# Performance work log

Hardware: AMD Instinct MI355X
Metric: run time of the kernel (lower is better)

Reference implementation:

```python
import jax, jax.numpy as jnp
import numpy as np
import math

D_MODEL = 1024
N_DEVICES = 64
HIDDEN = 128
N_HEADS = 8
B, S = 16, 1024
W_SCALE = 0.02

def setup_inputs() -> dict:
    key = jax.random.key(0)
    ks = jax.random.split(key, 24)
    f = jax.random.normal
    inp = {
        'x': f(ks[0], (B, S, D_MODEL), jnp.float32),
        # attention pooling (n_heads=8, non-causal, self-attention) weights, stored [in,out]
        'wq': f(ks[1], (D_MODEL, D_MODEL), jnp.float32) * W_SCALE,
        'bq': jnp.zeros((D_MODEL,), jnp.float32),
        'wk': f(ks[2], (D_MODEL, D_MODEL), jnp.float32) * W_SCALE,
        'bk': jnp.zeros((D_MODEL,), jnp.float32),
        'wv': f(ks[3], (D_MODEL, D_MODEL), jnp.float32) * W_SCALE,
        'bv': jnp.zeros((D_MODEL,), jnp.float32),
        'wo': f(ks[4], (D_MODEL, D_MODEL), jnp.float32) * W_SCALE,
        'bo': jnp.zeros((D_MODEL,), jnp.float32),
        # device embedding table
        'emb': f(ks[5], (N_DEVICES, D_MODEL), jnp.float32),
        # routing gate: Linear(2d,d) -> Tanh -> Linear(d,N) -> Softmax
        'rg_w1': f(ks[6], (2 * D_MODEL, D_MODEL), jnp.float32) * W_SCALE,
        'rg_b1': jnp.zeros((D_MODEL,), jnp.float32),
        'rg_w2': f(ks[7], (D_MODEL, N_DEVICES), jnp.float32) * W_SCALE,
        'rg_b2': jnp.zeros((N_DEVICES,), jnp.float32),
        'reg_w1': f(ks[8], (N_DEVICES, D_MODEL, HIDDEN), jnp.float32) * W_SCALE,
        'reg_b1': jnp.zeros((N_DEVICES, HIDDEN), jnp.float32),
        'reg_w2': f(ks[9], (N_DEVICES, HIDDEN), jnp.float32) * W_SCALE,
        'reg_b2': jnp.zeros((N_DEVICES,), jnp.float32),
        # stacked per-device classification heads: Linear(d,h)->ReLU->Linear(h,1)->Sigmoid
        'cls_w1': f(ks[10], (N_DEVICES, D_MODEL, HIDDEN), jnp.float32) * W_SCALE,
        'cls_b1': jnp.zeros((N_DEVICES, HIDDEN), jnp.float32),
        'cls_w2': f(ks[11], (N_DEVICES, HIDDEN), jnp.float32) * W_SCALE,
        'cls_b2': jnp.zeros((N_DEVICES,), jnp.float32),
    }
    return inp


def _forward(x, wq, bq, wk, bk, wv, bv, wo, bo, emb,
             rg_w1, rg_b1, rg_w2, rg_b2,
             reg_w1, reg_b1, reg_w2, reg_b2,
             cls_w1, cls_b1, cls_w2, cls_b2):
    b, s, d = x.shape
    dk = d // N_HEADS
    scale = 1.0 / math.sqrt(dk)

    def split_heads(t):  # [b,s,d] -> [b,h,s,dk]
        return t.reshape(b, s, N_HEADS, dk).transpose(0, 2, 1, 3)

    Q = split_heads(x @ wq + bq)
    K = split_heads(x @ wk + bk)
    V = split_heads(x @ wv + bv)
    scores = jnp.einsum('bhqd,bhkd->bhqk', Q, K) * scale
    attn = jax.nn.softmax(scores, axis=-1)  # non-causal, no mask, eval (no dropout)
    ctx = jnp.einsum('bhqk,bhkd->bhqd', attn, V)
    ctx = ctx.transpose(0, 2, 1, 3).reshape(b, s, d)
    pooled = ctx @ wo + bo                       # [b,s,d]
    g = pooled.mean(axis=1)                      # [b,d] global_repr

    g_exp = jnp.broadcast_to(g[:, None, :], (b, N_DEVICES, d))
    de_exp = jnp.broadcast_to(emb[None, :, :], (b, N_DEVICES, d))

    # routing gate
    ri = jnp.concatenate([g_exp, de_exp], axis=-1)        # [b,N,2d]
    h = jnp.tanh(ri @ rg_w1 + rg_b1)                      # [b,N,d]
    rw = jax.nn.softmax(h @ rg_w2 + rg_b2, axis=-1)       # [b,N,N]
    device_repr = jnp.einsum('bnm,md->bnd', rw, emb)      # bmm with expanded embeds
    combined = g_exp + device_repr                        # [b,N,d]

    hr = jax.nn.relu(jnp.einsum('bnd,ndh->bnh', combined, reg_w1) + reg_b1)
    reg = jax.nn.softplus(jnp.einsum('bnh,nh->bn', hr, reg_w2) + reg_b2)

    # per-device classification heads (stacked)
    hc = jax.nn.relu(jnp.einsum('bnd,ndh->bnh', combined, cls_w1) + cls_b1)
    cls = jax.nn.sigmoid(jnp.einsum('bnh,nh->bn', hc, cls_w2) + cls_b2)
    return reg, cls


def reference(x, wq, bq, wk, bk, wv, bv, wo, bo, emb,
              rg_w1, rg_b1, rg_w2, rg_b2,
              reg_w1, reg_b1, reg_w2, reg_b2,
              cls_w1, cls_b1, cls_w2, cls_b2):
    return _forward(x, wq, bq, wk, bk, wv, bv, wo, bo, emb,
                    rg_w1, rg_b1, rg_w2, rg_b2,
                    reg_w1, reg_b1, reg_w2, reg_b2,
                    cls_w1, cls_b1, cls_w2, cls_b2)
```

## Files before the change

kernel.cpp:

```cpp
#include <hip/hip_runtime.h>

typedef unsigned short ushort_t;
typedef __attribute__((ext_vector_type(8))) short short8;
typedef __attribute__((ext_vector_type(4))) float floatx4;

__device__ __forceinline__ ushort_t f2bf(float f) {
    unsigned u = __float_as_uint(f);
    return (ushort_t)((u + 0x7fffu + ((u >> 16) & 1u)) >> 16);
}
__device__ __forceinline__ void gll16(const void* g, void* l) {
    __builtin_amdgcn_global_load_lds(
        (const __attribute__((address_space(1))) unsigned int*)g,
        (__attribute__((address_space(3))) unsigned int*)l, 16, 0, 0);
}
#if __has_builtin(__builtin_amdgcn_exp2f)
#define EXP2f(x) __builtin_amdgcn_exp2f(x)
#else
#define EXP2f(x) exp2f(x)
#endif

__global__ __launch_bounds__(256) void prep_tr_kernel(
    const float* __restrict__ x, ushort_t* __restrict__ xb,
    const float* __restrict__ wq, const float* __restrict__ wk,
    ushort_t* __restrict__ wqT, ushort_t* __restrict__ wkT)
{
    __shared__ float t[64][65];
    const int bid = blockIdx.x;
    const int tid = threadIdx.x;
    if (bid < 8192) {
        size_t i = ((size_t)bid * 256 + tid) * 8;
        float4 v0 = *(const float4*)(x + i);
        float4 v1 = *(const float4*)(x + i + 4);
        uint4 o;
        o.x = (unsigned)f2bf(v0.x) | ((unsigned)f2bf(v0.y) << 16);
        o.y = (unsigned)f2bf(v0.z) | ((unsigned)f2bf(v0.w) << 16);
        o.z = (unsigned)f2bf(v1.x) | ((unsigned)f2bf(v1.y) << 16);
        o.w = (unsigned)f2bf(v1.z) | ((unsigned)f2bf(v1.w) << 16);
        *(uint4*)(xb + i) = o;
        return;
    }
    const int b2 = bid - 8192;
    const int bx = b2 & 15, by = (b2 >> 4) & 15, bz = b2 >> 8;
    const float* src = bz ? wk : wq;
    ushort_t* dst = bz ? wkT : wqT;
    const int k0 = bx * 64, n0 = by * 64;
    const int rr = tid >> 4, cc = (tid & 15) * 4;
#pragma unroll
    for (int p = 0; p < 4; ++p) {
        float4 v = *(const float4*)(src + (size_t)(k0 + p * 16 + rr) * 1024 + n0 + cc);
        t[p * 16 + rr][cc + 0] = v.x;
        t[p * 16 + rr][cc + 1] = v.y;
        t[p * 16 + rr][cc + 2] = v.z;
        t[p * 16 + rr][cc + 3] = v.w;
    }
    __syncthreads();
#pragma unroll
    for (int p = 0; p < 4; ++p) {
        int nl = p * 16 + rr;
        uint2 o;
        o.x = (unsigned)f2bf(t[cc + 0][nl]) | ((unsigned)f2bf(t[cc + 1][nl]) << 16);
        o.y = (unsigned)f2bf(t[cc + 2][nl]) | ((unsigned)f2bf(t[cc + 3][nl]) << 16);
        *(uint2*)(dst + (size_t)(n0 + nl) * 1024 + k0 + cc) = o;
    }
}

__global__ __launch_bounds__(512, 4) void gemm_qk_kernel(
    const ushort_t* __restrict__ xb, const ushort_t* __restrict__ wqT, const ushort_t* __restrict__ wkT,
    const float* __restrict__ bq, const float* __restrict__ bk,
    ushort_t* __restrict__ Qb, ushort_t* __restrict__ Kb)
{
    const int bm = blockIdx.x;
    const int bn = blockIdx.y;

    __shared__ ushort_t a_lds[2][128 * 32];
    __shared__ ushort_t q_lds[2][128 * 32];
    __shared__ ushort_t k_lds[2][128 * 32];

    const int tid = threadIdx.x;
    const int lane = tid & 63;
    const int wave = tid >> 6;
    const int wmat = wave >> 2;
    const int wr = (wave >> 1) & 1, wc = wave & 1;
    const int l16 = lane & 15, quad = lane >> 4;
    const int qs = quad ^ ((l16 >> 1) & 3);

    floatx4 acc[4][4];
    const floatx4 zero4 = {0.f, 0.f, 0.f, 0.f};
#pragma unroll
    for (int i = 0; i < 4; ++i)
#pragma unroll
        for (int j = 0; j < 4; ++j) acc[i][j] = zero4;

    const int srow = tid >> 2;
    const int skof = ((tid & 3) ^ ((tid >> 3) & 3)) * 8;
    const ushort_t* gA = xb + (size_t)(bm * 128 + srow) * 1024 + skof;
    const ushort_t* gQ = wqT + (size_t)(bn * 128 + srow) * 1024 + skof;
    const ushort_t* gK = wkT + (size_t)(bn * 128 + srow) * 1024 + skof;

    auto issue = [&](int buf, int k0) {
        gll16(gA + k0, &a_lds[buf][wave * 512]);
        gll16(gQ + k0, &q_lds[buf][wave * 512]);
        gll16(gK + k0, &k_lds[buf][wave * 512]);
    };

    const ushort_t* lbase = wmat ? k_lds[0] : q_lds[0];
    const int lstride = wmat ? (int)(k_lds[1] - k_lds[0]) : (int)(q_lds[1] - q_lds[0]);

    auto compute = [&](int buf) {
        const ushort_t* la = a_lds[buf];
        const ushort_t* lb = lbase + buf * lstride;
        short8 afr[4], bfr[4];
#pragma unroll
        for (int mi = 0; mi < 4; ++mi)
            afr[mi] = *(const short8*)&la[(wr * 64 + mi * 16 + l16) * 32 + qs * 8];
#pragma unroll
        for (int ni = 0; ni < 4; ++ni)
            bfr[ni] = *(const short8*)&lb[(wc * 64 + ni * 16 + l16) * 32 + qs * 8];
#pragma unroll
        for (int mi = 0; mi < 4; ++mi)
#pragma unroll
            for (int ni = 0; ni < 4; ++ni)
                acc[mi][ni] = __builtin_amdgcn_mfma_f32_16x16x32_bf16(afr[mi], bfr[ni], acc[mi][ni], 0, 0, 0);
    };

    issue(0, 0);
#pragma unroll 4
    for (int kt = 0; kt < 31; ++kt) {
        __syncthreads();
        issue((kt + 1) & 1, (kt + 1) * 32);
        compute(kt & 1);
    }
    __syncthreads();
    compute(1);

    ushort_t* Out = wmat ? Kb : Qb;
    const float* bias = wmat ? bk : bq;
    const float postscale = wmat ? 1.0f : 0.12751744900508692f;

    const int bq_ = bm >> 3;
    const int sb = (bm & 7) * 128 + wr * 64 + quad * 4;
    const int dc = wc * 64 + l16;
    float bp[4];
#pragma unroll
    for (int ni = 0; ni < 4; ++ni) bp[ni] = bias[bn * 128 + dc + ni * 16] * postscale;
    ushort_t* ob = Out + ((size_t)(bq_ * 8 + bn) * 1024 + sb) * 128 + dc;
#pragma unroll
    for (int mi = 0; mi < 4; ++mi)
#pragma unroll
        for (int ni = 0; ni < 4; ++ni) {
            ushort_t* p = ob + mi * 2048 + ni * 16;
#pragma unroll
            for (int r = 0; r < 4; ++r)
                p[r * 128] = f2bf(fmaf(acc[mi][ni][r], postscale, bp[ni]));
        }
}

__global__ __launch_bounds__(512, 4) void attn_mfma_kernel(
    const ushort_t* __restrict__ Qb,
    const ushort_t* __restrict__ Kb,
    float* __restrict__ wout)
{
    const int bh = blockIdx.x;
    const int qt = blockIdx.y;
    __shared__ ushort_t ks[2][64 * 128];

    const int tid = threadIdx.x;
    const int wave = tid >> 6, lane = tid & 63;
    const int l16 = lane & 15, quad = lane >> 4;

    const ushort_t* Ksrc = Kb + (size_t)bh * 1024 * 128;

    int srcoff[2];
#pragma unroll
    for (int c = 0; c < 2; ++c) {
        int r = c * 32 + (tid >> 4);
        int g = (tid & 15) ^ (r & 15);
        srcoff[c] = r * 128 + g * 8;
    }

    auto issue = [&](int buf, int kt) {
        const ushort_t* src = Ksrc + (size_t)kt * 8192;
#pragma unroll
        for (int c = 0; c < 2; ++c)
            gll16(src + srcoff[c], &ks[buf][c * 4096 + wave * 512]);
    };

    short8 aq[2][4];
    {
        const ushort_t* qsrc = Qb + ((size_t)bh * 1024 + qt * 256 + wave * 32) * 128;
#pragma unroll
        for (int mi = 0; mi < 2; ++mi)
#pragma unroll
            for (int ksp = 0; ksp < 4; ++ksp)
                aq[mi][ksp] = *(const short8*)(qsrc + (size_t)(mi * 16 + l16) * 128 + ksp * 32 + quad * 8);
    }

    const floatx4 zero4 = {0.f, 0.f, 0.f, 0.f};
    float lsum[2][4];
#pragma unroll
    for (int mi = 0; mi < 2; ++mi)
#pragma unroll
        for (int r = 0; r < 4; ++r) lsum[mi][r] = 0.f;

    issue(0, 0);

    for (int kt = 0; kt < 16; ++kt) {
        __syncthreads();
        if (kt < 15) issue((kt + 1) & 1, kt + 1);
        const ushort_t* kbuf = ks[kt & 1];
        floatx4 acc[2][4];
#pragma unroll
        for (int mi = 0; mi < 2; ++mi)
#pragma unroll
            for (int ni = 0; ni < 4; ++ni) acc[mi][ni] = zero4;
#pragma unroll
        for (int ksp = 0; ksp < 4; ++ksp) {
            short8 bk[4];
#pragma unroll
            for (int ni = 0; ni < 4; ++ni) {
                int n = ni * 16 + l16;
                int gs = (ksp * 4 + quad) ^ (n & 15);
                bk[ni] = *(const short8*)&kbuf[n * 128 + gs * 8];
            }
#pragma unroll
            for (int mi = 0; mi < 2; ++mi)
#pragma unroll
                for (int ni = 0; ni < 4; ++ni)
                    acc[mi][ni] = __builtin_amdgcn_mfma_f32_16x16x32_bf16(aq[mi][ksp], bk[ni], acc[mi][ni], 0, 0, 0);
        }
#pragma unroll
        for (int mi = 0; mi < 2; ++mi)
#pragma unroll
            for (int r = 0; r < 4; ++r) {
                float s = 0.f;
#pragma unroll
                for (int ni = 0; ni < 4; ++ni) s += EXP2f(acc[mi][ni][r]);
                lsum[mi][r] += s;
            }
    }

    issue(0, 0);

    float invl[2][4];
#pragma unroll
    for (int mi = 0; mi < 2; ++mi)
#pragma unroll
        for (int r = 0; r < 4; ++r) {
            float s = lsum[mi][r];
#pragma unroll
            for (int off = 1; off < 16; off <<= 1) s += __shfl_xor(s, off, 16);
            invl[mi][r] = 1.f / s;
        }

    for (int kt = 0; kt < 16; ++kt) {
        __syncthreads();
        if (kt < 15) issue((kt + 1) & 1, kt + 1);
        const ushort_t* kbuf = ks[kt & 1];
        floatx4 acc[2][4];
#pragma unroll
        for (int mi = 0; mi < 2; ++mi)
#pragma unroll
            for (int ni = 0; ni < 4; ++ni) acc[mi][ni] = zero4;
#pragma unroll
        for (int ksp = 0; ksp < 4; ++ksp) {
            short8 bk[4];
#pragma unroll
            for (int ni = 0; ni < 4; ++ni) {
                int n = ni * 16 + l16;
                int gs = (ksp * 4 + quad) ^ (n & 15);
                bk[ni] = *(const short8*)&kbuf[n * 128 + gs * 8];
            }
#pragma unroll
            for (int mi = 0; mi < 2; ++mi)
#pragma unroll
                for (int ni = 0; ni < 4; ++ni)
                    acc[mi][ni] = __builtin_amdgcn_mfma_f32_16x16x32_bf16(aq[mi][ksp], bk[ni], acc[mi][ni], 0, 0, 0);
        }
#pragma unroll
        for (int ni = 0; ni < 4; ++ni) {
            float s = 0.f;
#pragma unroll
            for (int mi = 0; mi < 2; ++mi)
#pragma unroll
                for (int r = 0; r < 4; ++r)
                    s += EXP2f(acc[mi][ni][r]) * invl[mi][r];
            s += __shfl_xor(s, 16, 64);
            s += __shfl_xor(s, 32, 64);
            if (quad == 0) atomicAdd(&wout[bh * 1024 + kt * 64 + ni * 16 + l16], s);
        }
    }
}

__global__ __launch_bounds__(256) void u_kernel(const ushort_t* __restrict__ xb,
                                                const float* __restrict__ w,
                                                float* __restrict__ u)
{
    const int b = blockIdx.x, dc = blockIdx.y;
    const int tid = threadIdx.x;
    const int kp = tid >> 4, dli = tid & 15;
    const int d0 = dc * 64;
    __shared__ float4 accl[16][8][16];

    float4 acc[8];
#pragma unroll
    for (int h = 0; h < 8; ++h) acc[h] = make_float4(0.f, 0.f, 0.f, 0.f);

    const ushort_t* Xp = xb + ((size_t)(b * 1024 + kp * 64)) * 1024 + d0 + dli * 4;
    const float* wb = w + b * 8192 + kp * 64;
    for (int k = 0; k < 64; ++k) {
        uint2 uv = *(const uint2*)(Xp + (size_t)k * 1024);
        float x0 = __uint_as_float(uv.x << 16);
        float x1 = __uint_as_float(uv.x & 0xffff0000u);
        float x2 = __uint_as_float(uv.y << 16);
        float x3 = __uint_as_float(uv.y & 0xffff0000u);
#pragma unroll
        for (int h = 0; h < 8; ++h) {
            float ww = wb[h * 1024 + k];
            acc[h].x = fmaf(ww, x0, acc[h].x);
            acc[h].y = fmaf(ww, x1, acc[h].y);
            acc[h].z = fmaf(ww, x2, acc[h].z);
            acc[h].w = fmaf(ww, x3, acc[h].w);
        }
    }
#pragma unroll
    for (int h = 0; h < 8; ++h) accl[kp][h][dli] = acc[h];
    __syncthreads();
    if (tid < 128) {
        const int h = tid >> 4, di = tid & 15;
        float4 s = accl[0][h][di];
#pragma unroll
        for (int k2 = 1; k2 < 16; ++k2) {
            float4 v = accl[k2][h][di];
            s.x += v.x; s.y += v.y; s.z += v.z; s.w += v.w;
        }
        *(float4*)&u[((size_t)(b * 8 + h)) * 1024 + d0 + di * 4] = s;
    }
}

__global__ __launch_bounds__(256) void sgemm_kernel(
    const float* __restrict__ A, int lda, long sAz,
    const float* __restrict__ Bm, int ldb, long sBz,
    const float* __restrict__ bias, long sBiasz,
    float* __restrict__ C, int ldc, long sCz,
    int M, int N, int K, float alpha, int nks)
{
    const int z = blockIdx.z;
    const int ks = blockIdx.x % nks;
    const int mt = blockIdx.x / nks;
    const int Kc = K / nks;
    A += (size_t)z * sAz;
    Bm += (size_t)z * sBz;
    C += (size_t)z * sCz;
    const float* bptr = bias ? bias + (size_t)z * sBiasz : nullptr;
    __shared__ float As[64 * 36];
    __shared__ float Bs[32 * 68];
    const int tid = threadIdx.x;
    const int row0 = mt * 64, col0 = blockIdx.y * 64;
    const int ty = tid >> 4, tx = tid & 15;
    float acc[4][4] = {};
    const int aflat = tid * 8;
    const int ar = aflat >> 5, ac = aflat & 31;
    const int br = aflat >> 6, bc = aflat & 63;
    for (int k0 = ks * Kc; k0 < (ks + 1) * Kc; k0 += 32) {
        __syncthreads();
        float4 va0 = make_float4(0.f, 0.f, 0.f, 0.f), va1 = va0;
        if (row0 + ar < M) {
            const float* src = A + (size_t)(row0 + ar) * lda + k0 + ac;
            va0 = *(const float4*)src;
            va1 = *(const float4*)(src + 4);
        }
        *(float4*)&As[ar * 36 + ac] = va0;
        *(float4*)&As[ar * 36 + ac + 4] = va1;
        {
            const float* srcb = Bm + (size_t)(k0 + br) * ldb + col0 + bc;
            *(float4*)&Bs[br * 68 + bc] = *(const float4*)srcb;
            *(float4*)&Bs[br * 68 + bc + 4] = *(const float4*)(srcb + 4);
        }
        __syncthreads();
#pragma unroll
        for (int kk = 0; kk < 32; ++kk) {
            float a0 = As[(ty * 4 + 0) * 36 + kk];
            float a1 = As[(ty * 4 + 1) * 36 + kk];
            float a2 = As[(ty * 4 + 2) * 36 + kk];
            float a3 = As[(ty * 4 + 3) * 36 + kk];
            float b0 = Bs[kk * 68 + tx * 4 + 0];
            float b1 = Bs[kk * 68 + tx * 4 + 1];
            float b2 = Bs[kk * 68 + tx * 4 + 2];
            float b3 = Bs[kk * 68 + tx * 4 + 3];
            acc[0][0] = fmaf(a0, b0, acc[0][0]); acc[0][1] = fmaf(a0, b1, acc[0][1]);
            acc[0][2] = fmaf(a0, b2, acc[0][2]); acc[0][3] = fmaf(a0, b3, acc[0][3]);
            acc[1][0] = fmaf(a1, b0, acc[1][0]); acc[1][1] = fmaf(a1, b1, acc[1][1]);
            acc[1][2] = fmaf(a1, b2, acc[1][2]); acc[1][3] = fmaf(a1, b3, acc[1][3]);
            acc[2][0] = fmaf(a2, b0, acc[2][0]); acc[2][1] = fmaf(a2, b1, acc[2][1]);
            acc[2][2] = fmaf(a2, b2, acc[2][2]); acc[2][3] = fmaf(a2, b3, acc[2][3]);
            acc[3][0] = fmaf(a3, b0, acc[3][0]); acc[3][1] = fmaf(a3, b1, acc[3][1]);
            acc[3][2] = fmaf(a3, b2, acc[3][2]); acc[3][3] = fmaf(a3, b3, acc[3][3]);
        }
    }
#pragma unroll
    for (int i = 0; i < 4; ++i) {
        int r = row0 + ty * 4 + i;
        if (r >= M) continue;
#pragma unroll
        for (int j = 0; j < 4; ++j) {
            int c = col0 + tx * 4 + j;
            float v = alpha * acc[i][j] + ((bptr && ks == 0) ? bptr[c] : 0.f);
            if (nks > 1) atomicAdd(&C[(size_t)r * ldc + c], v);
            else C[(size_t)r * ldc + c] = v;
        }
    }
}

__global__ __launch_bounds__(256) void sgemm_ge_ee_kernel(
    const float* __restrict__ gbuf, const float* __restrict__ emb,
    const float* __restrict__ rg_w1, float* __restrict__ Ge, float* __restrict__ Ee)
{
    const int z = blockIdx.z;
    const float* A = z ? emb : gbuf;
    const float* Bm = rg_w1 + (size_t)z * 1048576;
    float* C = z ? Ee : Ge;
    const int M = z ? 64 : 16;
    const int nks = 8, Kc = 128;
    const int ks = blockIdx.x % nks;
    __shared__ float As[64 * 36];
    __shared__ float Bs[32 * 68];
    const int tid = threadIdx.x;
    const int col0 = blockIdx.y * 64;
    const int ty = tid >> 4, tx = tid & 15;
    float acc[4][4] = {};
    const int aflat = tid * 8;
    const int ar = aflat >> 5, ac = aflat & 31;
    const int br = aflat >> 6, bc = aflat & 63;
    for (int k0 = ks * Kc; k0 < (ks + 1) * Kc; k0 += 32) {
        __syncthreads();
        float4 va0 = make_float4(0.f, 0.f, 0.f, 0.f), va1 = va0;
        if (ar < M) {
            const float* src = A + (size_t)ar * 1024 + k0 + ac;
            va0 = *(const float4*)src;
            va1 = *(const float4*)(src + 4);
        }
        *(float4*)&As[ar * 36 + ac] = va0;
        *(float4*)&As[ar * 36 + ac + 4] = va1;
        {
            const float* srcb = Bm + (size_t)(k0 + br) * 1024 + col0 + bc;
            *(float4*)&Bs[br * 68 + bc] = *(const float4*)srcb;
            *(float4*)&Bs[br * 68 + bc + 4] = *(const float4*)(srcb + 4);
        }
        __syncthreads();
#pragma unroll
        for (int kk = 0; kk < 32; ++kk) {
            float a0 = As[(ty * 4 + 0) * 36 + kk];
            float a1 = As[(ty * 4 + 1) * 36 + kk];
            float a2 = As[(ty * 4 + 2) * 36 + kk];
            float a3 = As[(ty * 4 + 3) * 36 + kk];
            float b0 = Bs[kk * 68 + tx * 4 + 0];
            float b1 = Bs[kk * 68 + tx * 4 + 1];
            float b2 = Bs[kk * 68 + tx * 4 + 2];
            float b3 = Bs[kk * 68 + tx * 4 + 3];
            acc[0][0] = fmaf(a0, b0, acc[0][0]); acc[0][1] = fmaf(a0, b1, acc[0][1]);
            acc[0][2] = fmaf(a0, b2, acc[0][2]); acc[0][3] = fmaf(a0, b3, acc[0][3]);
            acc[1][0] = fmaf(a1, b0, acc[1][0]); acc[1][1] = fmaf(a1, b1, acc[1][1]);
            acc[1][2] = fmaf(a1, b2, acc[1][2]); acc[1][3] = fmaf(a1, b3, acc[1][3]);
            acc[2][0] = fmaf(a2, b0, acc[2][0]); acc[2][1] = fmaf(a2, b1, acc[2][1]);
            acc[2][2] = fmaf(a2, b2, acc[2][2]); acc[2][3] = fmaf(a2, b3, acc[2][3]);
            acc[3][0] = fmaf(a3, b0, acc[3][0]); acc[3][1] = fmaf(a3, b1, acc[3][1]);
            acc[3][2] = fmaf(a3, b2, acc[3][2]); acc[3][3] = fmaf(a3, b3, acc[3][3]);
        }
    }
#pragma unroll
    for (int i = 0; i < 4; ++i) {
        int r = ty * 4 + i;
        if (r >= M) continue;
#pragma unroll
        for (int j = 0; j < 4; ++j) {
            int c = col0 + tx * 4 + j;
            atomicAdd(&C[(size_t)r * 1024 + c], acc[i][j]);
        }
    }
}

__global__ __launch_bounds__(256) void gate_kernel(
    const float* __restrict__ Ge, const float* __restrict__ Ee, const float* __restrict__ rg_b1,
    const float* __restrict__ rg_w2, const float* __restrict__ rg_b2,
    const float* __restrict__ emb, float* __restrict__ DR)
{
    const int row = blockIdx.x;
    const int b = row >> 6, n = row & 63;
    __shared__ float h[1024];
    __shared__ float red[256];
    __shared__ float rw[64];
    const int tid = threadIdx.x;
    for (int c = tid; c < 1024; c += 256)
        h[c] = tanhf(Ge[b * 1024 + c] + Ee[n * 1024 + c] + rg_b1[c]);
    __syncthreads();
    const int j = tid & 63, ch = tid >> 6;
    float part = 0.f;
    const float* w2p = rg_w2 + (size_t)(ch * 256) * 64 + j;
    for (int c = 0; c < 256; ++c)
        part = fmaf(h[ch * 256 + c], w2p[c * 64], part);
    red[tid] = part;
    __syncthreads();
    if (tid < 64) {
        float lg = red[tid] + red[tid + 64] + red[tid + 128] + red[tid + 192] + rg_b2[j];
        float m = lg;
#pragma unroll
        for (int off = 1; off < 64; off <<= 1) m = fmaxf(m, __shfl_xor(m, off, 64));
        float e = __expf(lg - m);
        float s = e;
#pragma unroll
        for (int off = 1; off < 64; off <<= 1) s += __shfl_xor(s, off, 64);
        rw[tid] = e / s;
    }
    __syncthreads();
    float4 acc = make_float4(0.f, 0.f, 0.f, 0.f);
    const float4* E4 = (const float4*)emb;
    for (int nn = 0; nn < 64; ++nn) {
        float wv = rw[nn];
        float4 ev = E4[nn * 256 + tid];
        acc.x = fmaf(wv, ev.x, acc.x);
        acc.y = fmaf(wv, ev.y, acc.y);
        acc.z = fmaf(wv, ev.z, acc.z);
        acc.w = fmaf(wv, ev.w, acc.w);
    }
    *(float4*)&DR[(size_t)row * 1024 + tid * 4] = acc;
}

__global__ __launch_bounds__(256) void heads_kernel(
    const float* __restrict__ g, const float* __restrict__ DR,
    const float* __restrict__ rw1, const float* __restrict__ cw1,
    const float* __restrict__ rb1, const float* __restrict__ rw2, const float* __restrict__ rb2,
    const float* __restrict__ cb1, const float* __restrict__ cw2, const float* __restrict__ cb2,
    float* __restrict__ out)
{
    const int n = blockIdx.x, task = blockIdx.y, bq = blockIdx.z;
    __shared__ float comb[4][1024];
    __shared__ float apart[2][4][128];
    const int tid = threadIdx.x;
#pragma unroll
    for (int i = 0; i < 4; ++i) {
        int idx = tid + i * 256;
        int bb = idx >> 8, c4 = idx & 255;
        int b = bq * 4 + bb;
        float4 gv = *(const float4*)&g[b * 1024 + c4 * 4];
        float4 dv = *(const float4*)&DR[((size_t)(b * 64 + n)) * 1024 + c4 * 4];
        *(float4*)&comb[bb][c4 * 4] = make_float4(gv.x + dv.x, gv.y + dv.y, gv.z + dv.z, gv.w + dv.w);
    }
    __syncthreads();
    const int j = tid & 127, sub = tid >> 7;
    const float* W1 = (task ? cw1 : rw1) + (size_t)n * 131072 + (size_t)sub * 512 * 128 + j;
    float a[4] = {};
    for (int c4 = 0; c4 < 128; ++c4) {
        const int cb = sub * 512 + c4 * 4;
        const float w0 = W1[(c4 * 4 + 0) * 128];
        const float w1 = W1[(c4 * 4 + 1) * 128];
        const float w2 = W1[(c4 * 4 + 2) * 128];
        const float w3 = W1[(c4 * 4 + 3) * 128];
#pragma unroll
        for (int bb = 0; bb < 4; ++bb) {
            float4 cv = *(const float4*)&comb[bb][cb];
            a[bb] = fmaf(cv.x, w0, a[bb]);
            a[bb] = fmaf(cv.y, w1, a[bb]);
            a[bb] = fmaf(cv.z, w2, a[bb]);
            a[bb] = fmaf(cv.w, w3, a[bb]);
        }
    }
#pragma unroll
    for (int bb = 0; bb < 4; ++bb) apart[sub][bb][j] = a[bb];
    __syncthreads();
    const int wv = tid >> 6, lane = tid & 63;
    const float* b1 = (task ? cb1 : rb1) + n * 128;
    const float* W2 = (task ? cw2 : rw2) + n * 128;
    float h1 = b1[lane]      + apart[0][wv][lane]      + apart[1][wv][lane];
    float h2 = b1[lane + 64] + apart[0][wv][lane + 64] + apart[1][wv][lane + 64];
    float s = fmaxf(h1, 0.f) * W2[lane] + fmaxf(h2, 0.f) * W2[lane + 64];
#pragma unroll
    for (int off = 1; off < 64; off <<= 1) s += __shfl_xor(s, off, 64);
    if (lane == 0) {
        s += (task ? cb2 : rb2)[n];
        float r = task ? (1.f / (1.f + __expf(-s)))
                       : (fmaxf(s, 0.f) + log1pf(__expf(-fabsf(s))));
        out[task * 1024 + (bq * 4 + wv) * 64 + n] = r;
    }
}

extern "C" void kernel_launch(void* const* d_in, const int* in_sizes, int n_in,
                              void* d_out, int out_size, void* d_ws, size_t ws_size,
                              hipStream_t stream)
{
    const float* x      = (const float*)d_in[0];
    const float* wq     = (const float*)d_in[1];
    const float* bq     = (const float*)d_in[2];
    const float* wk     = (const float*)d_in[3];
    const float* bk     = (const float*)d_in[4];
    const float* wv     = (const float*)d_in[5];
    const float* bv     = (const float*)d_in[6];
    const float* wo     = (const float*)d_in[7];
    const float* bo     = (const float*)d_in[8];
    const float* emb    = (const float*)d_in[9];
    const float* rg_w1  = (const float*)d_in[10];
    const float* rg_b1  = (const float*)d_in[11];
    const float* rg_w2  = (const float*)d_in[12];
    const float* rg_b2  = (const float*)d_in[13];
    const float* reg_w1 = (const float*)d_in[14];
    const float* reg_b1 = (const float*)d_in[15];
    const float* reg_w2 = (const float*)d_in[16];
    const float* reg_b2 = (const float*)d_in[17];
    const float* cls_w1 = (const float*)d_in[18];
    const float* cls_b1 = (const float*)d_in[19];
    const float* cls_w2 = (const float*)d_in[20];
    const float* cls_b2 = (const float*)d_in[21];

    char* ws = (char*)d_ws;
    size_t off = 0;
    auto alloc = [&](size_t bytes) { size_t cur = off; off += (bytes + 255) & ~(size_t)255; return cur; };

    ushort_t* xb  = (ushort_t*)(ws + alloc((size_t)16777216 * 2));
    ushort_t* wqT = (ushort_t*)(ws + alloc((size_t)1048576 * 2));
    ushort_t* wkT = (ushort_t*)(ws + alloc((size_t)1048576 * 2));
    ushort_t* Qb  = (ushort_t*)(ws + alloc((size_t)16777216 * 2));
    ushort_t* Kb  = (ushort_t*)(ws + alloc((size_t)16777216 * 2));
    size_t zero_beg = off;
    float* wcol = (float*)(ws + alloc((size_t)131072 * 4));
    float* cm   = (float*)(ws + alloc((size_t)16384 * 4));
    float* gbuf = (float*)(ws + alloc((size_t)16384 * 4));
    float* Ge   = (float*)(ws + alloc((size_t)16384 * 4));
    float* Ee   = (float*)(ws + alloc((size_t)65536 * 4));
    size_t zero_end = off;
    float* u    = (float*)(ws + alloc((size_t)131072 * 4));
    float* DR   = (float*)(ws + alloc((size_t)1048576 * 4));

    hipMemsetAsync(ws + zero_beg, 0, zero_end - zero_beg, stream);

    prep_tr_kernel<<<8704, 256, 0, stream>>>(x, xb, wq, wk, wqT, wkT);
    gemm_qk_kernel<<<dim3(128, 8), 512, 0, stream>>>(xb, wqT, wkT, bq, bk, Qb, Kb);
    attn_mfma_kernel<<<dim3(128, 4), 512, 0, stream>>>(Qb, Kb, wcol);
    u_kernel<<<dim3(16, 16), 256, 0, stream>>>(xb, wcol, u);
    sgemm_kernel<<<dim3(8, 2, 8), 256, 0, stream>>>(u, 8192, 1024, wv, 1024, 128, bv, 128,
                                                    cm, 1024, 128, 16, 128, 1024, 1.f / 1024.f, 8);
    sgemm_kernel<<<dim3(8, 16, 1), 256, 0, stream>>>(cm, 1024, 0, wo, 1024, 0, bo, 0,
                                                     gbuf, 1024, 0, 16, 1024, 1024, 1.f, 8);
    sgemm_ge_ee_kernel<<<dim3(8, 16, 2), 256, 0, stream>>>(gbuf, emb, rg_w1, Ge, Ee);
    gate_kernel<<<1024, 256, 0, stream>>>(Ge, Ee, rg_b1, rg_w2, rg_b2, emb, DR);
    heads_kernel<<<dim3(64, 2, 4), 256, 0, stream>>>(gbuf, DR, reg_w1, cls_w1,
                                                     reg_b1, reg_w2, reg_b2,
                                                     cls_b1, cls_w2, cls_b2, (float*)d_out);
    (void)in_sizes; (void)n_in; (void)out_size; (void)ws_size;
}
```

Measured before the change: 452.8 us.

## Hoist embedding-gate GEMM into prep kernel and batch gate rows per block

The emb @ rg_w1[d:] GEMM does not depend on the attention path, so it moves into the prep kernel as extra blocks and runs alongside the conversion and transpose work. The remaining Ge GEMM uses the generic sgemm kernel. The gate kernel now handles four rows per block, so each rg_w2 and emb load is reused four times and the grid shrinks from 1024 to 256 blocks. In exchange the prep kernel uses more shared memory and the gate kernel runs fewer blocks.

After: 451.6 us. Within noise of the previous version (-0.3%).

```diff
diff --git a/kernel.cpp b/kernel.cpp
--- a/kernel.cpp
+++ b/kernel.cpp
@@ -19,12 +19,74 @@
 #define EXP2f(x) exp2f(x)
 #endif
 
+
+__device__ __forceinline__ void sgemm_body(
+    const float* __restrict__ A, int lda, const float* __restrict__ Bm, int ldb,
+    const float* __restrict__ bias, float* __restrict__ C, int ldc,
+    int M, int Kc, int ks, int col0, float alpha,
+    int tid, float* As, float* Bs)
+{
+    const int ty = tid >> 4, tx = tid & 15;
+    float acc[4][4] = {};
+    const int aflat = tid * 8;
+    const int ar = aflat >> 5, ac = aflat & 31;
+    const int br = aflat >> 6, bc = aflat & 63;
+    for (int k0 = ks * Kc; k0 < (ks + 1) * Kc; k0 += 32) {
+        __syncthreads();
+        float4 va0 = make_float4(0.f, 0.f, 0.f, 0.f), va1 = va0;
+        if (ar < M) {
+            const float* src = A + (size_t)ar * lda + k0 + ac;
+            va0 = *(const float4*)src;
+            va1 = *(const float4*)(src + 4);
+        }
+        *(float4*)&As[ar * 36 + ac] = va0;
+        *(float4*)&As[ar * 36 + ac + 4] = va1;
+        {
+            const float* srcb = Bm + (size_t)(k0 + br) * ldb + col0 + bc;
+            *(float4*)&Bs[br * 68 + bc] = *(const float4*)srcb;
+            *(float4*)&Bs[br * 68 + bc + 4] = *(const float4*)(srcb + 4);
+        }
+        __syncthreads();
+#pragma unroll
+        for (int kk = 0; kk < 32; ++kk) {
+            float a0 = As[(ty * 4 + 0) * 36 + kk];
+            float a1 = As[(ty * 4 + 1) * 36 + kk];
+            float a2 = As[(ty * 4 + 2) * 36 + kk];
+            float a3 = As[(ty * 4 + 3) * 36 + kk];
+            float b0 = Bs[kk * 68 + tx * 4 + 0];
+            float b1 = Bs[kk * 68 + tx * 4 + 1];
+            float b2 = Bs[kk * 68 + tx * 4 + 2];
+            float b3 = Bs[kk * 68 + tx * 4 + 3];
+            acc[0][0] = fmaf(a0, b0, acc[0][0]); acc[0][1] = fmaf(a0, b1, acc[0][1]);
+            acc[0][2] = fmaf(a0, b2, acc[0][2]); acc[0][3] = fmaf(a0, b3, acc[0][3]);
+            acc[1][0] = fmaf(a1, b0, acc[1][0]); acc[1][1] = fmaf(a1, b1, acc[1][1]);
+            acc[1][2] = fmaf(a1, b2, acc[1][2]); acc[1][3] = fmaf(a1, b3, acc[1][3]);
+            acc[2][0] = fmaf(a2, b0, acc[2][0]); acc[2][1] = fmaf(a2, b1, acc[2][1]);
+            acc[2][2] = fmaf(a2, b2, acc[2][2]); acc[2][3] = fmaf(a2, b3, acc[2][3]);
+            acc[3][0] = fmaf(a3, b0, acc[3][0]); acc[3][1] = fmaf(a3, b1, acc[3][1]);
+            acc[3][2] = fmaf(a3, b2, acc[3][2]); acc[3][3] = fmaf(a3, b3, acc[3][3]);
+        }
+    }
+#pragma unroll
+    for (int i = 0; i < 4; ++i) {
+        int r = ty * 4 + i;
+        if (r >= M) continue;
+#pragma unroll
+        for (int j = 0; j < 4; ++j) {
+            int c = col0 + tx * 4 + j;
+            float v = alpha * acc[i][j] + ((bias && ks == 0) ? bias[c] : 0.f);
+            atomicAdd(&C[(size_t)r * ldc + c], v);
+        }
+    }
+}
+
 __global__ __launch_bounds__(256) void prep_tr_kernel(
     const float* __restrict__ x, ushort_t* __restrict__ xb,
     const float* __restrict__ wq, const float* __restrict__ wk,
-    ushort_t* __restrict__ wqT, ushort_t* __restrict__ wkT)
-{
-    __shared__ float t[64][65];
+    ushort_t* __restrict__ wqT, ushort_t* __restrict__ wkT,
+    const float* __restrict__ emb, const float* __restrict__ rg_w1, float* __restrict__ Ee)
+{
+    __shared__ __align__(16) char psm[18432];
     const int bid = blockIdx.x;
     const int tid = threadIdx.x;
     if (bid < 8192) {
@@ -39,29 +101,39 @@
         *(uint4*)(xb + i) = o;
         return;
     }
-    const int b2 = bid - 8192;
-    const int bx = b2 & 15, by = (b2 >> 4) & 15, bz = b2 >> 8;
-    const float* src = bz ? wk : wq;
-    ushort_t* dst = bz ? wkT : wqT;
-    const int k0 = bx * 64, n0 = by * 64;
-    const int rr = tid >> 4, cc = (tid & 15) * 4;
-#pragma unroll
-    for (int p = 0; p < 4; ++p) {
-        float4 v = *(const float4*)(src + (size_t)(k0 + p * 16 + rr) * 1024 + n0 + cc);
-        t[p * 16 + rr][cc + 0] = v.x;
-        t[p * 16 + rr][cc + 1] = v.y;
-        t[p * 16 + rr][cc + 2] = v.z;
-        t[p * 16 + rr][cc + 3] = v.w;
-    }
-    __syncthreads();
-#pragma unroll
-    for (int p = 0; p < 4; ++p) {
-        int nl = p * 16 + rr;
-        uint2 o;
-        o.x = (unsigned)f2bf(t[cc + 0][nl]) | ((unsigned)f2bf(t[cc + 1][nl]) << 16);
-        o.y = (unsigned)f2bf(t[cc + 2][nl]) | ((unsigned)f2bf(t[cc + 3][nl]) << 16);
-        *(uint2*)(dst + (size_t)(n0 + nl) * 1024 + k0 + cc) = o;
-    }
+    if (bid < 8704) {
+        float (*t)[65] = (float(*)[65])psm;
+        const int b2 = bid - 8192;
+        const int bx = b2 & 15, by = (b2 >> 4) & 15, bz = b2 >> 8;
+        const float* src = bz ? wk : wq;
+        ushort_t* dst = bz ? wkT : wqT;
+        const int k0 = bx * 64, n0 = by * 64;
+        const int rr = tid >> 4, cc = (tid & 15) * 4;
+#pragma unroll
+        for (int p = 0; p < 4; ++p) {
+            float4 v = *(const float4*)(src + (size_t)(k0 + p * 16 + rr) * 1024 + n0 + cc);
+            t[p * 16 + rr][cc + 0] = v.x;
+            t[p * 16 + rr][cc + 1] = v.y;
+            t[p * 16 + rr][cc + 2] = v.z;
+            t[p * 16 + rr][cc + 3] = v.w;
+        }
+        __syncthreads();
+#pragma unroll
+        for (int p = 0; p < 4; ++p) {
+            int nl = p * 16 + rr;
+            uint2 o;
+            o.x = (unsigned)f2bf(t[cc + 0][nl]) | ((unsigned)f2bf(t[cc + 1][nl]) << 16);
+            o.y = (unsigned)f2bf(t[cc + 2][nl]) | ((unsigned)f2bf(t[cc + 3][nl]) << 16);
+            *(uint2*)(dst + (size_t)(n0 + nl) * 1024 + k0 + cc) = o;
+        }
+        return;
+    }
+    float* As = (float*)psm;
+    float* Bs = As + 64 * 36;
+    const int bx2 = bid - 8704;
+    const int ks = bx2 & 7, coly = bx2 >> 3;
+    sgemm_body(emb, 1024, rg_w1 + (size_t)1048576, 1024, nullptr,
+               Ee, 1024, 64, 128, ks, coly * 64, 1.f, tid, As, Bs);
 }
 
 __global__ __launch_bounds__(512, 4) void gemm_qk_kernel(
@@ -411,118 +483,67 @@
     }
 }
 
-__global__ __launch_bounds__(256) void sgemm_ge_ee_kernel(
-    const float* __restrict__ gbuf, const float* __restrict__ emb,
-    const float* __restrict__ rg_w1, float* __restrict__ Ge, float* __restrict__ Ee)
-{
-    const int z = blockIdx.z;
-    const float* A = z ? emb : gbuf;
-    const float* Bm = rg_w1 + (size_t)z * 1048576;
-    float* C = z ? Ee : Ge;
-    const int M = z ? 64 : 16;
-    const int nks = 8, Kc = 128;
-    const int ks = blockIdx.x % nks;
-    __shared__ float As[64 * 36];
-    __shared__ float Bs[32 * 68];
-    const int tid = threadIdx.x;
-    const int col0 = blockIdx.y * 64;
-    const int ty = tid >> 4, tx = tid & 15;
-    float acc[4][4] = {};
-    const int aflat = tid * 8;
-    const int ar = aflat >> 5, ac = aflat & 31;
-    const int br = aflat >> 6, bc = aflat & 63;
-    for (int k0 = ks * Kc; k0 < (ks + 1) * Kc; k0 += 32) {
-        __syncthreads();
-        float4 va0 = make_float4(0.f, 0.f, 0.f, 0.f), va1 = va0;
-        if (ar < M) {
-            const float* src = A + (size_t)ar * 1024 + k0 + ac;
-            va0 = *(const float4*)src;
-            va1 = *(const float4*)(src + 4);
-        }
-        *(float4*)&As[ar * 36 + ac] = va0;
-        *(float4*)&As[ar * 36 + ac + 4] = va1;
-        {
-            const float* srcb = Bm + (size_t)(k0 + br) * 1024 + col0 + bc;
-            *(float4*)&Bs[br * 68 + bc] = *(const float4*)srcb;
-            *(float4*)&Bs[br * 68 + bc + 4] = *(const float4*)(srcb + 4);
-        }
-        __syncthreads();
-#pragma unroll
-        for (int kk = 0; kk < 32; ++kk) {
-            float a0 = As[(ty * 4 + 0) * 36 + kk];
-            float a1 = As[(ty * 4 + 1) * 36 + kk];
-            float a2 = As[(ty * 4 + 2) * 36 + kk];
-            float a3 = As[(ty * 4 + 3) * 36 + kk];
-            float b0 = Bs[kk * 68 + tx * 4 + 0];
-            float b1 = Bs[kk * 68 + tx * 4 + 1];
-            float b2 = Bs[kk * 68 + tx * 4 + 2];
-            float b3 = Bs[kk * 68 + tx * 4 + 3];
-            acc[0][0] = fmaf(a0, b0, acc[0][0]); acc[0][1] = fmaf(a0, b1, acc[0][1]);
-            acc[0][2] = fmaf(a0, b2, acc[0][2]); acc[0][3] = fmaf(a0, b3, acc[0][3]);
-            acc[1][0] = fmaf(a1, b0, acc[1][0]); acc[1][1] = fmaf(a1, b1, acc[1][1]);
-            acc[1][2] = fmaf(a1, b2, acc[1][2]); acc[1][3] = fmaf(a1, b3, acc[1][3]);
-            acc[2][0] = fmaf(a2, b0, acc[2][0]); acc[2][1] = fmaf(a2, b1, acc[2][1]);
-            acc[2][2] = fmaf(a2, b2, acc[2][2]); acc[2][3] = fmaf(a2, b3, acc[2][3]);
-            acc[3][0] = fmaf(a3, b0, acc[3][0]); acc[3][1] = fmaf(a3, b1, acc[3][1]);
-            acc[3][2] = fmaf(a3, b2, acc[3][2]); acc[3][3] = fmaf(a3, b3, acc[3][3]);
-        }
-    }
-#pragma unroll
-    for (int i = 0; i < 4; ++i) {
-        int r = ty * 4 + i;
-        if (r >= M) continue;
-#pragma unroll
-        for (int j = 0; j < 4; ++j) {
-            int c = col0 + tx * 4 + j;
-            atomicAdd(&C[(size_t)r * 1024 + c], acc[i][j]);
-        }
-    }
-}
-
 __global__ __launch_bounds__(256) void gate_kernel(
     const float* __restrict__ Ge, const float* __restrict__ Ee, const float* __restrict__ rg_b1,
     const float* __restrict__ rg_w2, const float* __restrict__ rg_b2,
     const float* __restrict__ emb, float* __restrict__ DR)
 {
-    const int row = blockIdx.x;
-    const int b = row >> 6, n = row & 63;
-    __shared__ float h[1024];
-    __shared__ float red[256];
-    __shared__ float rw[64];
+    const int row0 = blockIdx.x * 4;
+    const int b = row0 >> 6, n0 = row0 & 63;
+    __shared__ float h[4][1024];
+    __shared__ float red[4][256];
+    __shared__ float rw[4][64];
     const int tid = threadIdx.x;
-    for (int c = tid; c < 1024; c += 256)
-        h[c] = tanhf(Ge[b * 1024 + c] + Ee[n * 1024 + c] + rg_b1[c]);
+    for (int idx = tid; idx < 4096; idx += 256) {
+        int rr = idx >> 10, c = idx & 1023;
+        h[rr][c] = tanhf(Ge[b * 1024 + c] + Ee[(n0 + rr) * 1024 + c] + rg_b1[c]);
+    }
     __syncthreads();
     const int j = tid & 63, ch = tid >> 6;
-    float part = 0.f;
+    float part[4] = {0.f, 0.f, 0.f, 0.f};
     const float* w2p = rg_w2 + (size_t)(ch * 256) * 64 + j;
-    for (int c = 0; c < 256; ++c)
-        part = fmaf(h[ch * 256 + c], w2p[c * 64], part);
-    red[tid] = part;
+    for (int c = 0; c < 256; ++c) {
+        float w = w2p[c * 64];
+#pragma unroll
+        for (int rr = 0; rr < 4; ++rr)
+            part[rr] = fmaf(h[rr][ch * 256 + c], w, part[rr]);
+    }
+#pragma unroll
+    for (int rr = 0; rr < 4; ++rr) red[rr][tid] = part[rr];
     __syncthreads();
     if (tid < 64) {
-        float lg = red[tid] + red[tid + 64] + red[tid + 128] + red[tid + 192] + rg_b2[j];
-        float m = lg;
-#pragma unroll
-        for (int off = 1; off < 64; off <<= 1) m = fmaxf(m, __shfl_xor(m, off, 64));
-        float e = __expf(lg - m);
-        float s = e;
-#pragma unroll
-        for (int off = 1; off < 64; off <<= 1) s += __shfl_xor(s, off, 64);
-        rw[tid] = e / s;
+#pragma unroll
+        for (int rr = 0; rr < 4; ++rr) {
+            float lg = red[rr][tid] + red[rr][tid + 64] + red[rr][tid + 128] + red[rr][tid + 192] + rg_b2[j];
+            float m = lg;
+#pragma unroll
+            for (int off = 1; off < 64; off <<= 1) m = fmaxf(m, __shfl_xor(m, off, 64));
+            float e = __expf(lg - m);
+            float s = e;
+#pragma unroll
+            for (int off = 1; off < 64; off <<= 1) s += __shfl_xor(s, off, 64);
+            rw[rr][tid] = e / s;
+        }
     }
     __syncthreads();
-    float4 acc = make_float4(0.f, 0.f, 0.f, 0.f);
+    float4 acc[4];
+#pragma unroll
+    for (int rr = 0; rr < 4; ++rr) acc[rr] = make_float4(0.f, 0.f, 0.f, 0.f);
     const float4* E4 = (const float4*)emb;
     for (int nn = 0; nn < 64; ++nn) {
-        float wv = rw[nn];
         float4 ev = E4[nn * 256 + tid];
-        acc.x = fmaf(wv, ev.x, acc.x);
-        acc.y = fmaf(wv, ev.y, acc.y);
-        acc.z = fmaf(wv, ev.z, acc.z);
-        acc.w = fmaf(wv, ev.w, acc.w);
-    }
-    *(float4*)&DR[(size_t)row * 1024 + tid * 4] = acc;
+#pragma unroll
+        for (int rr = 0; rr < 4; ++rr) {
+            float wv = rw[rr][nn];
+            acc[rr].x = fmaf(wv, ev.x, acc[rr].x);
+            acc[rr].y = fmaf(wv, ev.y, acc[rr].y);
+            acc[rr].z = fmaf(wv, ev.z, acc[rr].z);
+            acc[rr].w = fmaf(wv, ev.w, acc[rr].w);
+        }
+    }
+#pragma unroll
+    for (int rr = 0; rr < 4; ++rr)
+        *(float4*)&DR[(size_t)(row0 + rr) * 1024 + tid * 4] = acc[rr];
 }
 
 __global__ __launch_bounds__(256) void heads_kernel(
@@ -631,7 +652,7 @@
 
     hipMemsetAsync(ws + zero_beg, 0, zero_end - zero_beg, stream);
 
-    prep_tr_kernel<<<8704, 256, 0, stream>>>(x, xb, wq, wk, wqT, wkT);
+    prep_tr_kernel<<<8832, 256, 0, stream>>>(x, xb, wq, wk, wqT, wkT, emb, rg_w1, Ee);
     gemm_qk_kernel<<<dim3(128, 8), 512, 0, stream>>>(xb, wqT, wkT, bq, bk, Qb, Kb);
     attn_mfma_kernel<<<dim3(128, 4), 512, 0, stream>>>(Qb, Kb, wcol);
     u_kernel<<<dim3(16, 16), 256, 0, stream>>>(xb, wcol, u);
@@ -639,8 +660,9 @@
                                                     cm, 1024, 128, 16, 128, 1024, 1.f / 1024.f, 8);
     sgemm_kernel<<<dim3(8, 16, 1), 256, 0, stream>>>(cm, 1024, 0, wo, 1024, 0, bo, 0,
                                                      gbuf, 1024, 0, 16, 1024, 1024, 1.f, 8);
-    sgemm_ge_ee_kernel<<<dim3(8, 16, 2), 256, 0, stream>>>(gbuf, emb, rg_w1, Ge, Ee);
-    gate_kernel<<<1024, 256, 0, stream>>>(Ge, Ee, rg_b1, rg_w2, rg_b2, emb, DR);
+    sgemm_kernel<<<dim3(8, 16, 1), 256, 0, stream>>>(gbuf, 1024, 0, rg_w1, 1024, 0, nullptr, 0,
+                                                     Ge, 1024, 0, 16, 1024, 1024, 1.f, 8);
+    gate_kernel<<<256, 256, 0, stream>>>(Ge, Ee, rg_b1, rg_w2, rg_b2, emb, DR);
     heads_kernel<<<dim3(64, 2, 4), 256, 0, stream>>>(gbuf, DR, reg_w1, cls_w1,
                                                      reg_b1, reg_w2, reg_b2,
                                                      cls_b1, cls_w2, cls_b2, (float*)d_out);
```
